# Kernel optimization log

Measured on AMD Instinct MI355X. Metric: run time of the kernel, lower is better.

The kernel has to match this reference:

```python
import jax, jax.numpy as jnp
import numpy as np

N_E = 1024
N_H = 16
SZ = N_E // N_H  # 64
NEG_INF = float('-inf')


def _layernorm(x, g, b):
    # Faithful to source: unbiased variance (ddof=1), eps added AFTER sqrt.
    mu = jnp.mean(x, axis=-1, keepdims=True)
    v = jnp.var(x, axis=-1, keepdims=True, ddof=1)
    xn = (x - mu) / (jnp.sqrt(v) + 1e-8)
    return g * xn + b


def setup_inputs() -> dict:
    key = jax.random.key(0)
    ks = jax.random.split(key, 16)
    s = 0.02
    x = jax.random.normal(ks[0], (4, 2048, N_E), dtype=jnp.float32)
    # Stacked per-head Q/K/V linears: weight [H, sz, n_e], bias [H, sz]
    Wq = jax.random.normal(ks[1], (N_H, SZ, N_E), dtype=jnp.float32) * s
    bq = jax.random.normal(ks[2], (N_H, SZ), dtype=jnp.float32) * s
    Wk = jax.random.normal(ks[3], (N_H, SZ, N_E), dtype=jnp.float32) * s
    bk = jax.random.normal(ks[4], (N_H, SZ), dtype=jnp.float32) * s
    Wv = jax.random.normal(ks[5], (N_H, SZ, N_E), dtype=jnp.float32) * s
    bv = jax.random.normal(ks[6], (N_H, SZ), dtype=jnp.float32) * s
    Wo = jax.random.normal(ks[7], (N_E, N_E), dtype=jnp.float32) * s
    bo = jax.random.normal(ks[8], (N_E,), dtype=jnp.float32) * s
    g1 = jnp.ones((N_E,), dtype=jnp.float32)
    be1 = jnp.zeros((N_E,), dtype=jnp.float32)
    g2 = jnp.ones((N_E,), dtype=jnp.float32)
    be2 = jnp.zeros((N_E,), dtype=jnp.float32)
    W1 = jax.random.normal(ks[9], (4 * N_E, N_E), dtype=jnp.float32) * s
    bf1 = jax.random.normal(ks[10], (4 * N_E,), dtype=jnp.float32) * s
    W2 = jax.random.normal(ks[11], (N_E, 4 * N_E), dtype=jnp.float32) * s
    bf2 = jax.random.normal(ks[12], (N_E,), dtype=jnp.float32) * s
    return dict(x=x, Wq=Wq, bq=bq, Wk=Wk, bk=bk, Wv=Wv, bv=bv, Wo=Wo, bo=bo,
                g1=g1, be1=be1, g2=g2, be2=be2, W1=W1, bf1=bf1, W2=W2, bf2=bf2)


def reference(x, Wq, bq, Wk, bk, Wv, bv, Wo, bo, g1, be1, g2, be2, W1, bf1, W2, bf2):
    # --- MHA sublayer ---
    xn = _layernorm(x, g1, be1)
    # Q/K/V for all heads at once: [B, H, S, sz]
    Q = jnp.einsum('bsd,hkd->bhsk', xn, Wq) + bq[None, :, None, :]
    K = jnp.einsum('bsd,hkd->bhsk', xn, Wk) + bk[None, :, None, :]
    V = jnp.einsum('bsd,hkd->bhsk', xn, Wv) + bv[None, :, None, :]
    scores = jnp.einsum('bhqk,bhmk->bhqm', Q, K) / (SZ ** 0.5)  # [B,H,S,S]
    # Faithful to source quirk: mask where tril(scores) == 0
    masked = jnp.where(jnp.tril(scores) == 0, NEG_INF, scores)
    attn = jax.nn.softmax(masked, axis=-1)
    o = jnp.einsum('bhqm,bhmk->bhqk', attn, V)  # [B,H,S,sz]
    B, H, S, _ = o.shape
    o = jnp.transpose(o, (0, 2, 1, 3)).reshape(B, S, H * SZ)  # concat heads
    x = x + o @ Wo.T + bo
    # --- FFN sublayer (dropout = identity in eval) ---
    xn2 = _layernorm(x, g2, be2)
    h = jax.nn.gelu(xn2 @ W1.T + bf1, approximate=False)
    x = x + h @ W2.T + bf2
    return x
```

## Files before the change

kernel.cpp:

```cpp
#include <hip/hip_runtime.h>
#include <math.h>


typedef unsigned short u16;
typedef unsigned int u32;
typedef __attribute__((ext_vector_type(8))) short bf16x8;
typedef __attribute__((ext_vector_type(4))) float f32x4;

#define T_TOK 8192
#define DM    1024
#define SEQ   2048
#define PST   88
#define TST   136

__device__ __forceinline__ u16 f2bf(float f) {
  union { float f; unsigned int u; } c; c.f = f;
  unsigned int u = c.u + 0x7fffu + ((c.u >> 16) & 1u);
  return (u16)(u >> 16);
}

__device__ __forceinline__ u32 pk2(float a, float b) {
  return (u32)f2bf(a) | ((u32)f2bf(b) << 16);
}

__device__ __forceinline__ float bf2f(short s) {
  union { float f; unsigned int u; } c; c.u = ((u32)(u16)s) << 16;
  return c.f;
}

__device__ __forceinline__ void gload16(const void* gp, void* lp) {
  __builtin_amdgcn_global_load_lds(
      (const __attribute__((address_space(1))) void*)gp,
      (__attribute__((address_space(3))) void*)lp, 16, 0, 0);
}

__device__ __forceinline__ float gelu_tanh(float v) {
  float u = 0.7978845608f * (v + 0.044715f * v * v * v);
  return v / (1.0f + __expf(-2.0f * u));
}

__global__ __launch_bounds__(256) void prep_kernel(
    const float* __restrict__ x, const float* __restrict__ g,
    const float* __restrict__ b, u16* __restrict__ xnB,
    const float* __restrict__ Wq, const float* __restrict__ Wk,
    const float* __restrict__ Wv, const float* __restrict__ Wo,
    const float* __restrict__ W1, const float* __restrict__ W2,
    u16* __restrict__ WqkvB, u16* __restrict__ WoB,
    u16* __restrict__ W1B, u16* __restrict__ W2B,
    const float* __restrict__ bq, const float* __restrict__ bk,
    const float* __restrict__ bv, float* __restrict__ bqkv) {
  __shared__ float red[4];
  const int bid = blockIdx.x, tid = threadIdx.x;
  if (bid < 8192) {
    const int l = tid & 63, w = tid >> 6;
    const size_t row = bid;
    float4 v = reinterpret_cast<const float4*>(x + row * DM)[tid];
    float s = v.x + v.y + v.z + v.w;
#pragma unroll
    for (int off = 1; off < 64; off <<= 1) s += __shfl_xor(s, off, 64);
    if (l == 0) red[w] = s;
    __syncthreads();
    float mu = (red[0] + red[1] + red[2] + red[3]) * (1.0f / 1024.0f);
    float dx = v.x - mu, dy = v.y - mu, dz = v.z - mu, dw = v.w - mu;
    float ss = dx * dx + dy * dy + dz * dz + dw * dw;
#pragma unroll
    for (int off = 1; off < 64; off <<= 1) ss += __shfl_xor(ss, off, 64);
    __syncthreads();
    if (l == 0) red[w] = ss;
    __syncthreads();
    float var = (red[0] + red[1] + red[2] + red[3]) * (1.0f / 1023.0f);
    float inv = 1.0f / (sqrtf(var) + 1e-8f);
    const int c = tid * 4;
    u16* o = xnB + row * DM + c;
    o[0] = f2bf(dx * inv * g[c + 0] + b[c + 0]);
    o[1] = f2bf(dy * inv * g[c + 1] + b[c + 1]);
    o[2] = f2bf(dz * inv * g[c + 2] + b[c + 2]);
    o[3] = f2bf(dw * inv * g[c + 3] + b[c + 3]);
  } else if (bid < 10240) {
    for (int i = (bid - 8192) * 256 + tid; i < 3145728; i += 2048 * 256) {
      const float* s; u16* d; int j;
      if (i < 262144)       { s = Wq; d = WqkvB;           j = i; }
      else if (i < 524288)  { s = Wk; d = WqkvB + 1048576; j = i - 262144; }
      else if (i < 786432)  { s = Wv; d = WqkvB + 2097152; j = i - 524288; }
      else if (i < 1048576) { s = Wo; d = WoB;             j = i - 786432; }
      else if (i < 2097152) { s = W1; d = W1B;             j = i - 1048576; }
      else                  { s = W2; d = W2B;             j = i - 2097152; }
      float4 v = reinterpret_cast<const float4*>(s)[j];
      ushort4 o = { f2bf(v.x), f2bf(v.y), f2bf(v.z), f2bf(v.w) };
      reinterpret_cast<ushort4*>(d)[j] = o;
    }
  } else {
    int i = (bid - 10240) * 256 + tid;
    float val = (i < 1024) ? bq[i] : (i < 2048) ? bk[i - 1024] : bv[i - 2048];
    bqkv[i] = val;
  }
}

__global__ __launch_bounds__(256) void ln_kernel_b(const u16* __restrict__ x,
    const float* __restrict__ g, const float* __restrict__ b, u16* __restrict__ out) {
  __shared__ float red[4];
  const int tid = threadIdx.x, l = tid & 63, w = tid >> 6;
  const size_t row = blockIdx.x;
  ushort4 raw = reinterpret_cast<const ushort4*>(x + row * DM)[tid];
  float vx = bf2f((short)raw.x), vy = bf2f((short)raw.y);
  float vz = bf2f((short)raw.z), vw = bf2f((short)raw.w);
  float s = vx + vy + vz + vw;
#pragma unroll
  for (int off = 1; off < 64; off <<= 1) s += __shfl_xor(s, off, 64);
  if (l == 0) red[w] = s;
  __syncthreads();
  float mu = (red[0] + red[1] + red[2] + red[3]) * (1.0f / 1024.0f);
  float dx = vx - mu, dy = vy - mu, dz = vz - mu, dw = vw - mu;
  float ss = dx * dx + dy * dy + dz * dz + dw * dw;
#pragma unroll
  for (int off = 1; off < 64; off <<= 1) ss += __shfl_xor(ss, off, 64);
  __syncthreads();
  if (l == 0) red[w] = ss;
  __syncthreads();
  float var = (red[0] + red[1] + red[2] + red[3]) * (1.0f / 1023.0f);
  float inv = 1.0f / (sqrtf(var) + 1e-8f);
  const int c = tid * 4;
  u16* o = out + row * DM + c;
  o[0] = f2bf(dx * inv * g[c + 0] + b[c + 0]);
  o[1] = f2bf(dy * inv * g[c + 1] + b[c + 1]);
  o[2] = f2bf(dz * inv * g[c + 2] + b[c + 2]);
  o[3] = f2bf(dw * inv * g[c + 3] + b[c + 3]);
}

template <int EPI, int BM>
__global__ __launch_bounds__(512) void gemm8p(const u16* __restrict__ A,
    const u16* __restrict__ Bw, const float* __restrict__ bias,
    const float* res, void* Cout, void* aux, int M, int N, int K, int gx) {
  constexpr int MI  = BM / 32;
  constexpr int AMI = MI / 2;
  constexpr int VC  = (BM == 256) ? 6 : 5;
  __shared__ __align__(16) u16 shm[BM * 128 + 256 * 128];
  const int tid = threadIdx.x;
  const int l = tid & 63;
  const int w = tid >> 6;
  const int wm = w >> 2, wn = w & 3;
  const int lr = l & 15, lg = l >> 4;

  const int nb = gridDim.x;
  const int q = nb >> 3, r = nb & 7;
  const int xcd = blockIdx.x & 7, jj = blockIdx.x >> 3;
  const int lid = (xcd < r ? xcd * (q + 1) : r * (q + 1) + (xcd - r) * q) + jj;
  const int stid = lid >> 5, pos = lid & 31;
  const int nstx = gx >> 2;
  const int stx = stid % nstx, sty = stid / nstx;
  const int bx = stx * 4 + (pos & 3), by = sty * 8 + (pos >> 2);
  const int m0 = by * BM, n0 = bx * 256;

  const int Dl = tid * 16;
  const int Ls = Dl ^ (((Dl >> 7) & 3) << 4);
  const int srow = Ls >> 6;
  const int scol = (Ls & 63) >> 1;
  const u16* aS0 = A  + (size_t)(m0 + srow) * K + scol;
  const u16* aS1 = aS0 + (size_t)128 * K;
  const u16* bS0 = Bw + (size_t)(n0 + srow) * K + scol;
  const u16* bS1 = bS0 + (size_t)128 * K;

  const int sx = ((lr >> 1) & 3) << 4;
  const int aBase = (wm * (BM / 2) + lr) * 64 + ((lg * 16) ^ sx);
  const int bBase = (wn * 64 + lr) * 64 + ((lg * 16) ^ sx);

  f32x4 acc[MI][4];
#pragma unroll
  for (int i = 0; i < MI; ++i)
#pragma unroll
    for (int j = 0; j < 4; ++j) acc[i][j] = f32x4{0.f, 0.f, 0.f, 0.f};
  bf16x8 bv[2][4];

  const int NT = K >> 6;
  const int NI = NT >> 1;

  auto stA = [&](int d, int ks, int tile) {
    u16* dst = shm + (d * 2 + ks) * (BM * 32) + tid * 8;
    const int ko = tile * 64 + ks * 32;
    gload16(aS0 + ko, dst);
    if constexpr (BM == 256) gload16(aS1 + ko, dst + 4096);
  };
  auto stB = [&](int d, int ks, int tile) {
    u16* dst = shm + BM * 128 + (d * 2 + ks) * (256 * 32) + tid * 8;
    const int ko = tile * 64 + ks * 32;
    gload16(bS0 + ko, dst);
    gload16(bS1 + ko, dst + 4096);
  };

  stB(0, 0, 0); stB(0, 1, 0); stA(0, 0, 0); stA(0, 1, 0);
  stB(1, 0, 1); stB(1, 1, 1); stA(1, 0, 1);
  asm volatile("s_waitcnt vmcnt(%0)" :: "i"(VC) : "memory");
  __builtin_amdgcn_sched_barrier(0);
  __builtin_amdgcn_s_barrier();

#define PHASE(DBUF, KS, MH, READB, STAGE, ENDV)                               \
  {                                                                           \
    const char* abuf = (const char*)(shm + ((DBUF) * 2 + (KS)) * (BM * 32));  \
    const char* bbuf =                                                        \
        (const char*)(shm + BM * 128 + ((DBUF) * 2 + (KS)) * (256 * 32));     \
    bf16x8 av[AMI];                                                           \
    _Pragma("unroll")                                                         \
    for (int i = 0; i < AMI; ++i)                                             \
      av[i] = *(const bf16x8*)(abuf + aBase + ((MH) * AMI + i) * 1024);       \
    if (READB) {                                                              \
      _Pragma("unroll")                                                       \
      for (int ni = 0; ni < 4; ++ni)                                          \
        bv[KS][ni] = *(const bf16x8*)(bbuf + bBase + ni * 1024);              \
    }                                                                         \
    STAGE;                                                                    \
    __builtin_amdgcn_s_barrier();                                             \
    asm volatile("s_waitcnt lgkmcnt(0)" ::: "memory");                        \
    __builtin_amdgcn_sched_barrier(0);                                        \
    __builtin_amdgcn_s_setprio(1);                                            \
    _Pragma("unroll")                                                         \
    for (int i = 0; i < AMI; ++i)                                             \
      _Pragma("unroll")                                                       \
      for (int ni = 0; ni < 4; ++ni)                                          \
        acc[(MH) * AMI + i][ni] = __builtin_amdgcn_mfma_f32_16x16x32_bf16(    \
            av[i], bv[KS][ni], acc[(MH) * AMI + i][ni], 0, 0, 0);             \
    __builtin_amdgcn_s_setprio(0);                                            \
    ENDV;                                                                     \
    __builtin_amdgcn_s_barrier();                                             \
  }

#define ENDV_CNT                                                              \
  {                                                                           \
    if (t + 1 < NI) {                                                         \
      asm volatile("s_waitcnt vmcnt(%0)" :: "i"(VC) : "memory");              \
    } else {                                                                  \
      asm volatile("s_waitcnt vmcnt(0)" ::: "memory");                        \
    }                                                                         \
    __builtin_amdgcn_sched_barrier(0);                                        \
  }

  for (int t = 0; t < NI; ++t) {
    const int t2 = 2 * t;
    const bool s0 = (t2 + 2 < NT);
    const bool s1 = (t2 + 3 < NT);
    PHASE(0, 0, 0, 1, { stA(1, 1, t2 + 1); }, {});
    PHASE(0, 1, 0, 1, { if (s0) stB(0, 0, t2 + 2); }, {});
    PHASE(0, 0, 1, 0, { if (s0) stB(0, 1, t2 + 2); }, {});
    PHASE(0, 1, 1, 0, { if (s0) stA(0, 0, t2 + 2); }, ENDV_CNT);
    PHASE(1, 0, 0, 1, { if (s0) stA(0, 1, t2 + 2); }, {});
    PHASE(1, 1, 0, 1, { if (s1) stB(1, 0, t2 + 3); }, {});
    PHASE(1, 0, 1, 0, { if (s1) stB(1, 1, t2 + 3); }, {});
    PHASE(1, 1, 1, 0, { if (s1) stA(1, 0, t2 + 3); }, ENDV_CNT);
  }
#undef PHASE
#undef ENDV_CNT

  float bs[4];
#pragma unroll
  for (int ni = 0; ni < 4; ++ni) bs[ni] = bias[n0 + wn * 64 + ni * 16 + lr];

  if constexpr (EPI == 0) {
    if (n0 >= 2048) {
      u16* ldsT = shm;
#pragma unroll
      for (int mi = 0; mi < MI; ++mi)
#pragma unroll
        for (int ni = 0; ni < 4; ++ni) {
          const int c = wn * 64 + ni * 16 + lr;
          const int r0 = wm * (BM / 2) + mi * 16 + lg * 4;
          ushort4 pk = { f2bf(acc[mi][ni][0] + bs[ni]),
                         f2bf(acc[mi][ni][1] + bs[ni]),
                         f2bf(acc[mi][ni][2] + bs[ni]),
                         f2bf(acc[mi][ni][3] + bs[ni]) };
          *(ushort4*)&ldsT[c * TST + r0] = pk;
        }
      __syncthreads();
      const int b0 = m0 >> 11, s0b = m0 & 2047;
      const int cc = tid >> 1, hf = tid & 1;
      const int hd = (n0 - 2048) + cc, hh = hd >> 6, dd = hd & 63;
      u16* dst = (u16*)aux +
                 (((size_t)(b0 * 16 + hh) * 64 + dd) << 11) + s0b + hf * 64;
      const u16* srcT = &ldsT[cc * TST + hf * 64];
#pragma unroll
      for (int i2 = 0; i2 < 8; ++i2)
        *(bf16x8*)(dst + i2 * 8) = *(const bf16x8*)(srcT + i2 * 8);
      return;
    }
  }

#pragma unroll
  for (int mi = 0; mi < MI; ++mi) {
#pragma unroll
    for (int j = 0; j < 4; ++j) {
      const int rr = m0 + wm * (BM / 2) + mi * 16 + lg * 4 + j;
#pragma unroll
      for (int ni = 0; ni < 4; ++ni) {
        const int c = n0 + wn * 64 + ni * 16 + lr;
        float v = acc[mi][ni][j] + bs[ni];
        if constexpr (EPI == 0) {
          ((u16*)Cout)[(size_t)rr * 2048 + c] = f2bf(v);
        } else if constexpr (EPI == 1) {
          const size_t idx = (size_t)rr * N + c;
          ((u16*)Cout)[idx] = f2bf(v + res[idx]);
        } else if constexpr (EPI == 2) {
          const size_t idx = (size_t)rr * N + c;
          ((u16*)Cout)[idx] = f2bf(gelu_tanh(v));
        } else {
          const size_t idx = (size_t)rr * N + c;
          ((float*)Cout)[idx] = v + bf2f((short)((const u16*)res)[idx]);
        }
      }
    }
  }
}

__global__ __launch_bounds__(512) void attn_kernel(const u16* __restrict__ qk,
    const u16* __restrict__ vt, u16* __restrict__ obuf) {
  __shared__ __align__(16) u16 ldsK[6][64 * 64];
  __shared__ __align__(16) u16 ldsV[6][64 * 64];
  __shared__ __align__(16) u16 ldsP[8][2][16 * PST];
  const int tid = threadIdx.x, l = tid & 63, w = tid >> 6;
  const int lr = l & 15, lg = l >> 4;
  const int lid = (blockIdx.x & 7) * 32 + (blockIdx.x >> 3);
  const int bh = lid >> 2, bx = lid & 3;
  const int b = bh >> 4, h = bh & 15;
  const u16* qbase = qk + (size_t)b * SEQ * 2048 + h * 64;
  const u16* kbase = qk + (size_t)b * SEQ * 2048 + 1024 + h * 64;
  const u16* vbase = vt + (size_t)bh * 64 * SEQ;

  const int srow = tid >> 3;
  const int scb  = ((tid & 7) * 16) ^ ((srow & 7) << 4);
  const int sel  = scb >> 1;

  auto stageKV = [&](int t) {
    const int bi = t % 6;
    gload16(kbase + (size_t)(t * 64 + srow) * 2048 + sel, &ldsK[bi][tid * 8]);
    gload16(vbase + (size_t)srow * SEQ + t * 64 + sel,    &ldsV[bi][tid * 8]);
  };

#pragma unroll
  for (int half = 0; half < 2; ++half) {
    const int qt = half ? (7 - bx) : bx;
    const int q0 = qt * 256 + w * 32;
    bf16x8 qf[2][2];
#pragma unroll
    for (int mi = 0; mi < 2; ++mi)
#pragma unroll
      for (int ks = 0; ks < 2; ++ks) {
        bf16x8 raw = *(const bf16x8*)(qbase +
            (size_t)(q0 + mi * 16 + lr) * 2048 + ks * 32 + lg * 8);
        bf16x8 sc8;
#pragma unroll
        for (int i = 0; i < 8; ++i) sc8[i] = (short)f2bf(bf2f(raw[i]) * 0.125f);
        qf[mi][ks] = sc8;
      }

    f32x4 o[2][4];
#pragma unroll
    for (int mi = 0; mi < 2; ++mi)
#pragma unroll
      for (int nd = 0; nd < 4; ++nd) o[mi][nd] = f32x4{0.f, 0.f, 0.f, 0.f};
    float m_[2] = {-1e30f, -1e30f}, ls[2] = {0.f, 0.f};

    const int nt = 4 * qt + 4;
    const int nip = nt >> 1;
    const int qmaxw = q0 + 31;

    stageKV(0); stageKV(1);

    for (int jt = 0; jt < nip; ++jt) {
      const int k0t = 2 * jt;
      if (jt + 1 < nip) {
        stageKV(k0t + 2); stageKV(k0t + 3);
        asm volatile("s_waitcnt vmcnt(4)" ::: "memory");
      } else {
        asm volatile("s_waitcnt vmcnt(0)" ::: "memory");
      }
      __builtin_amdgcn_s_barrier();
      __builtin_amdgcn_sched_barrier(0);

#pragma unroll
      for (int sub = 0; sub < 2; ++sub) {
        const int kt = k0t + sub;
        const u16* bK = &ldsK[kt % 6][0];
        const u16* bV = &ldsV[kt % 6][0];

        if (kt * 64 <= qmaxw) {
          f32x4 sc[2][4];
#pragma unroll
          for (int mi = 0; mi < 2; ++mi)
#pragma unroll
            for (int ni = 0; ni < 4; ++ni) sc[mi][ni] = f32x4{0.f, 0.f, 0.f, 0.f};
#pragma unroll
          for (int ks = 0; ks < 2; ++ks)
#pragma unroll
            for (int ni = 0; ni < 4; ++ni) {
              const int r2 = ni * 16 + lr;
              const int cb = (r2 << 7) + ((ks * 64 + lg * 16) ^ ((r2 & 7) << 4));
              bf16x8 kf = *(const bf16x8*)&bK[cb >> 1];
              sc[0][ni] = __builtin_amdgcn_mfma_f32_16x16x32_bf16(kf, qf[0][ks], sc[0][ni], 0, 0, 0);
              sc[1][ni] = __builtin_amdgcn_mfma_f32_16x16x32_bf16(kf, qf[1][ks], sc[1][ni], 0, 0, 0);
            }

          if (kt * 64 + 63 > q0) {
#pragma unroll
            for (int mi = 0; mi < 2; ++mi) {
              const int qa = q0 + mi * 16 + lr;
#pragma unroll
              for (int ni = 0; ni < 4; ++ni)
#pragma unroll
                for (int j = 0; j < 4; ++j) {
                  const int ka = kt * 64 + ni * 16 + lg * 4 + j;
                  if (ka > qa) sc[mi][ni][j] = -1e30f;
                }
            }
          }

#pragma unroll
          for (int mi = 0; mi < 2; ++mi) {
            float mx = sc[mi][0][0];
#pragma unroll
            for (int ni = 0; ni < 4; ++ni)
#pragma unroll
              for (int j = 0; j < 4; ++j) mx = fmaxf(mx, sc[mi][ni][j]);
            mx = fmaxf(mx, __shfl_xor(mx, 16, 64));
            mx = fmaxf(mx, __shfl_xor(mx, 32, 64));
            if (!__all(mx <= m_[mi] + 8.0f)) {
              const float newm = fmaxf(m_[mi], mx);
              const float alpha = __expf(m_[mi] - newm);
              m_[mi] = newm;
              ls[mi] *= alpha;
#pragma unroll
              for (int nd = 0; nd < 4; ++nd) {
                o[mi][nd][0] *= alpha; o[mi][nd][1] *= alpha;
                o[mi][nd][2] *= alpha; o[mi][nd][3] *= alpha;
              }
            }
            float ps = 0.f;
#pragma unroll
            for (int ni = 0; ni < 4; ++ni) {
              float p0 = __expf(sc[mi][ni][0] - m_[mi]);
              float p1 = __expf(sc[mi][ni][1] - m_[mi]);
              float p2 = __expf(sc[mi][ni][2] - m_[mi]);
              float p3 = __expf(sc[mi][ni][3] - m_[mi]);
              ps += (p0 + p1) + (p2 + p3);
              u32 w0 = pk2(p0, p1), w1 = pk2(p2, p3);
              *(uint2*)&ldsP[w][mi][lr * PST + ni * 16 + lg * 4] = make_uint2(w0, w1);
            }
            ps += __shfl_xor(ps, 16, 64);
            ps += __shfl_xor(ps, 32, 64);
            ls[mi] += ps;
          }

#pragma unroll
          for (int ks = 0; ks < 2; ++ks) {
            bf16x8 pf0 = *(const bf16x8*)&ldsP[w][0][lr * PST + ks * 32 + lg * 8];
            bf16x8 pf1 = *(const bf16x8*)&ldsP[w][1][lr * PST + ks * 32 + lg * 8];
#pragma unroll
            for (int nd = 0; nd < 4; ++nd) {
              const int r2 = nd * 16 + lr;
              const int cb = (r2 << 7) + ((ks * 64 + lg * 16) ^ ((r2 & 7) << 4));
              bf16x8 vf = *(const bf16x8*)&bV[cb >> 1];
              o[0][nd] = __builtin_amdgcn_mfma_f32_16x16x32_bf16(vf, pf0, o[0][nd], 0, 0, 0);
              o[1][nd] = __builtin_amdgcn_mfma_f32_16x16x32_bf16(vf, pf1, o[1][nd], 0, 0, 0);
            }
          }
        }
      }
    }
    __builtin_amdgcn_s_barrier();

#pragma unroll
    for (int mi = 0; mi < 2; ++mi) {
      const float inv = 1.0f / ls[mi];
      const int qrow = q0 + mi * 16 + lr;
      u16* op = obuf + (size_t)(b * SEQ + qrow) * DM + h * 64 + lg * 4;
#pragma unroll
      for (int nd = 0; nd < 4; ++nd) {
        ushort4 pk = { f2bf(o[mi][nd][0] * inv), f2bf(o[mi][nd][1] * inv),
                       f2bf(o[mi][nd][2] * inv), f2bf(o[mi][nd][3] * inv) };
        *(ushort4*)(op + nd * 16) = pk;
      }
    }
  }
}

extern "C" void kernel_launch(void* const* d_in, const int* in_sizes, int n_in,
                              void* d_out, int out_size, void* d_ws, size_t ws_size,
                              hipStream_t stream) {
  const float* x   = (const float*)d_in[0];
  const float* Wq  = (const float*)d_in[1];
  const float* bq  = (const float*)d_in[2];
  const float* Wk  = (const float*)d_in[3];
  const float* bk  = (const float*)d_in[4];
  const float* Wv  = (const float*)d_in[5];
  const float* bv  = (const float*)d_in[6];
  const float* Wo  = (const float*)d_in[7];
  const float* bo  = (const float*)d_in[8];
  const float* g1  = (const float*)d_in[9];
  const float* be1 = (const float*)d_in[10];
  const float* g2  = (const float*)d_in[11];
  const float* be2 = (const float*)d_in[12];
  const float* W1  = (const float*)d_in[13];
  const float* bf1 = (const float*)d_in[14];
  const float* W2  = (const float*)d_in[15];
  const float* bf2 = (const float*)d_in[16];
  float* out = (float*)d_out;

  char* ws = (char*)d_ws;
  size_t off = 0;
  auto alloc = [&](size_t bytes) {
    char* p = ws + off;
    off += (bytes + 255) & ~(size_t)255;
    return p;
  };
  u16* xnB = (u16*)alloc((size_t)T_TOK * DM * 2);
  u16* D    = (u16*)alloc((size_t)T_TOK * 4096 * 2);
  u16* qkB  = D;
  u16* VTg  = D + (size_t)T_TOK * 2048;
  u16* oB   = D + (size_t)T_TOK * 3072;
  u16* HB   = D;
  u16*   WqkvB = (u16*)alloc((size_t)3072 * 1024 * 2);
  u16*   WoB   = (u16*)alloc((size_t)1024 * 1024 * 2);
  u16*   W1B   = (u16*)alloc((size_t)4096 * 1024 * 2);
  u16*   W2B   = (u16*)alloc((size_t)1024 * 4096 * 2);
  u16*   x1B   = (u16*)alloc((size_t)T_TOK * DM * 2);
  float* bqkv  = (float*)alloc(3072 * 4);

  prep_kernel<<<10252, 256, 0, stream>>>(x, g1, be1, xnB,
                                         Wq, Wk, Wv, Wo, W1, W2,
                                         WqkvB, WoB, W1B, W2B,
                                         bq, bk, bv, bqkv);

  gemm8p<0, 128><<<768, 512, 0, stream>>>(xnB, WqkvB, bqkv, nullptr,
                                          qkB, VTg, T_TOK, 3072, 1024, 12);
  attn_kernel<<<256, 512, 0, stream>>>(qkB, VTg, oB);
  gemm8p<1, 128><<<256, 512, 0, stream>>>(oB, WoB, bo, x,
                                          x1B, nullptr, T_TOK, 1024, 1024, 4);

  ln_kernel_b<<<T_TOK, 256, 0, stream>>>(x1B, g2, be2, xnB);
  gemm8p<2, 256><<<512, 512, 0, stream>>>(xnB, W1B, bf1, nullptr,
                                          HB, nullptr, T_TOK, 4096, 1024, 16);
  gemm8p<3, 128><<<256, 512, 0, stream>>>(HB, W2B, bf2, (const float*)x1B,
                                          out, nullptr, T_TOK, 1024, 4096, 4);
}
```

Before: 344.6 us.

## Load K/V fragments directly from global memory instead of LDS staging

Drops the six-stage shared-memory ring buffer for K and V tiles, along with its async staging loads, waitcnt calls and workgroup barriers. Each wave now reads its K and V MFMA fragments straight from global memory, relying on L1/L2 caching for reuse across the 8 waves. This removes barrier synchronisation and LDS traffic, and each wave now breaks out at its own causal limit. In exchange it loses the prefetch pipelining and the sharing of loads across waves, which may expose global memory latency.

Measured after the change: 416.2 us. 20.8% more time.

```diff
diff --git a/kernel.cpp b/kernel.cpp
--- a/kernel.cpp
+++ b/kernel.cpp
@@ -310,8 +310,6 @@
 
 __global__ __launch_bounds__(512) void attn_kernel(const u16* __restrict__ qk,
     const u16* __restrict__ vt, u16* __restrict__ obuf) {
-  __shared__ __align__(16) u16 ldsK[6][64 * 64];
-  __shared__ __align__(16) u16 ldsV[6][64 * 64];
   __shared__ __align__(16) u16 ldsP[8][2][16 * PST];
   const int tid = threadIdx.x, l = tid & 63, w = tid >> 6;
   const int lr = l & 15, lg = l >> 4;
@@ -322,15 +320,7 @@
   const u16* kbase = qk + (size_t)b * SEQ * 2048 + 1024 + h * 64;
   const u16* vbase = vt + (size_t)bh * 64 * SEQ;
 
-  const int srow = tid >> 3;
-  const int scb  = ((tid & 7) * 16) ^ ((srow & 7) << 4);
-  const int sel  = scb >> 1;
-
-  auto stageKV = [&](int t) {
-    const int bi = t % 6;
-    gload16(kbase + (size_t)(t * 64 + srow) * 2048 + sel, &ldsK[bi][tid * 8]);
-    gload16(vbase + (size_t)srow * SEQ + t * 64 + sel,    &ldsV[bi][tid * 8]);
-  };
+  const int kcol = lg * 8;
 
 #pragma unroll
   for (int half = 0; half < 2; ++half) {
@@ -357,112 +347,91 @@
     float m_[2] = {-1e30f, -1e30f}, ls[2] = {0.f, 0.f};
 
     const int nt = 4 * qt + 4;
-    const int nip = nt >> 1;
     const int qmaxw = q0 + 31;
 
-    stageKV(0); stageKV(1);
-
-    for (int jt = 0; jt < nip; ++jt) {
-      const int k0t = 2 * jt;
-      if (jt + 1 < nip) {
-        stageKV(k0t + 2); stageKV(k0t + 3);
-        asm volatile("s_waitcnt vmcnt(4)" ::: "memory");
-      } else {
-        asm volatile("s_waitcnt vmcnt(0)" ::: "memory");
+    for (int kt = 0; kt < nt; ++kt) {
+      if (kt * 64 > qmaxw) break;
+
+      f32x4 sc[2][4];
+#pragma unroll
+      for (int mi = 0; mi < 2; ++mi)
+#pragma unroll
+        for (int ni = 0; ni < 4; ++ni) sc[mi][ni] = f32x4{0.f, 0.f, 0.f, 0.f};
+#pragma unroll
+      for (int ks = 0; ks < 2; ++ks)
+#pragma unroll
+        for (int ni = 0; ni < 4; ++ni) {
+          const int r2 = ni * 16 + lr;
+          bf16x8 kf = *(const bf16x8*)(kbase +
+              (size_t)(kt * 64 + r2) * 2048 + ks * 32 + kcol);
+          sc[0][ni] = __builtin_amdgcn_mfma_f32_16x16x32_bf16(kf, qf[0][ks], sc[0][ni], 0, 0, 0);
+          sc[1][ni] = __builtin_amdgcn_mfma_f32_16x16x32_bf16(kf, qf[1][ks], sc[1][ni], 0, 0, 0);
+        }
+
+      if (kt * 64 + 63 > q0) {
+#pragma unroll
+        for (int mi = 0; mi < 2; ++mi) {
+          const int qa = q0 + mi * 16 + lr;
+#pragma unroll
+          for (int ni = 0; ni < 4; ++ni)
+#pragma unroll
+            for (int j = 0; j < 4; ++j) {
+              const int ka = kt * 64 + ni * 16 + lg * 4 + j;
+              if (ka > qa) sc[mi][ni][j] = -1e30f;
+            }
+        }
       }
-      __builtin_amdgcn_s_barrier();
-      __builtin_amdgcn_sched_barrier(0);
-
-#pragma unroll
-      for (int sub = 0; sub < 2; ++sub) {
-        const int kt = k0t + sub;
-        const u16* bK = &ldsK[kt % 6][0];
-        const u16* bV = &ldsV[kt % 6][0];
-
-        if (kt * 64 <= qmaxw) {
-          f32x4 sc[2][4];
-#pragma unroll
-          for (int mi = 0; mi < 2; ++mi)
-#pragma unroll
-            for (int ni = 0; ni < 4; ++ni) sc[mi][ni] = f32x4{0.f, 0.f, 0.f, 0.f};
-#pragma unroll
-          for (int ks = 0; ks < 2; ++ks)
-#pragma unroll
-            for (int ni = 0; ni < 4; ++ni) {
-              const int r2 = ni * 16 + lr;
-              const int cb = (r2 << 7) + ((ks * 64 + lg * 16) ^ ((r2 & 7) << 4));
-              bf16x8 kf = *(const bf16x8*)&bK[cb >> 1];
-              sc[0][ni] = __builtin_amdgcn_mfma_f32_16x16x32_bf16(kf, qf[0][ks], sc[0][ni], 0, 0, 0);
-              sc[1][ni] = __builtin_amdgcn_mfma_f32_16x16x32_bf16(kf, qf[1][ks], sc[1][ni], 0, 0, 0);
-            }
-
-          if (kt * 64 + 63 > q0) {
-#pragma unroll
-            for (int mi = 0; mi < 2; ++mi) {
-              const int qa = q0 + mi * 16 + lr;
-#pragma unroll
-              for (int ni = 0; ni < 4; ++ni)
-#pragma unroll
-                for (int j = 0; j < 4; ++j) {
-                  const int ka = kt * 64 + ni * 16 + lg * 4 + j;
-                  if (ka > qa) sc[mi][ni][j] = -1e30f;
-                }
-            }
+
+#pragma unroll
+      for (int mi = 0; mi < 2; ++mi) {
+        float mx = sc[mi][0][0];
+#pragma unroll
+        for (int ni = 0; ni < 4; ++ni)
+#pragma unroll
+          for (int j = 0; j < 4; ++j) mx = fmaxf(mx, sc[mi][ni][j]);
+        mx = fmaxf(mx, __shfl_xor(mx, 16, 64));
+        mx = fmaxf(mx, __shfl_xor(mx, 32, 64));
+        if (!__all(mx <= m_[mi] + 8.0f)) {
+          const float newm = fmaxf(m_[mi], mx);
+          const float alpha = __expf(m_[mi] - newm);
+          m_[mi] = newm;
+          ls[mi] *= alpha;
+#pragma unroll
+          for (int nd = 0; nd < 4; ++nd) {
+            o[mi][nd][0] *= alpha; o[mi][nd][1] *= alpha;
+            o[mi][nd][2] *= alpha; o[mi][nd][3] *= alpha;
           }
-
-#pragma unroll
-          for (int mi = 0; mi < 2; ++mi) {
-            float mx = sc[mi][0][0];
-#pragma unroll
-            for (int ni = 0; ni < 4; ++ni)
-#pragma unroll
-              for (int j = 0; j < 4; ++j) mx = fmaxf(mx, sc[mi][ni][j]);
-            mx = fmaxf(mx, __shfl_xor(mx, 16, 64));
-            mx = fmaxf(mx, __shfl_xor(mx, 32, 64));
-            if (!__all(mx <= m_[mi] + 8.0f)) {
-              const float newm = fmaxf(m_[mi], mx);
-              const float alpha = __expf(m_[mi] - newm);
-              m_[mi] = newm;
-              ls[mi] *= alpha;
-#pragma unroll
-              for (int nd = 0; nd < 4; ++nd) {
-                o[mi][nd][0] *= alpha; o[mi][nd][1] *= alpha;
-                o[mi][nd][2] *= alpha; o[mi][nd][3] *= alpha;
-              }
-            }
-            float ps = 0.f;
-#pragma unroll
-            for (int ni = 0; ni < 4; ++ni) {
-              float p0 = __expf(sc[mi][ni][0] - m_[mi]);
-              float p1 = __expf(sc[mi][ni][1] - m_[mi]);
-              float p2 = __expf(sc[mi][ni][2] - m_[mi]);
-              float p3 = __expf(sc[mi][ni][3] - m_[mi]);
-              ps += (p0 + p1) + (p2 + p3);
-              u32 w0 = pk2(p0, p1), w1 = pk2(p2, p3);
-              *(uint2*)&ldsP[w][mi][lr * PST + ni * 16 + lg * 4] = make_uint2(w0, w1);
-            }
-            ps += __shfl_xor(ps, 16, 64);
-            ps += __shfl_xor(ps, 32, 64);
-            ls[mi] += ps;
-          }
-
-#pragma unroll
-          for (int ks = 0; ks < 2; ++ks) {
-            bf16x8 pf0 = *(const bf16x8*)&ldsP[w][0][lr * PST + ks * 32 + lg * 8];
-            bf16x8 pf1 = *(const bf16x8*)&ldsP[w][1][lr * PST + ks * 32 + lg * 8];
-#pragma unroll
-            for (int nd = 0; nd < 4; ++nd) {
-              const int r2 = nd * 16 + lr;
-              const int cb = (r2 << 7) + ((ks * 64 + lg * 16) ^ ((r2 & 7) << 4));
-              bf16x8 vf = *(const bf16x8*)&bV[cb >> 1];
-              o[0][nd] = __builtin_amdgcn_mfma_f32_16x16x32_bf16(vf, pf0, o[0][nd], 0, 0, 0);
-              o[1][nd] = __builtin_amdgcn_mfma_f32_16x16x32_bf16(vf, pf1, o[1][nd], 0, 0, 0);
-            }
-          }
+        }
+        float ps = 0.f;
+#pragma unroll
+        for (int ni = 0; ni < 4; ++ni) {
+          float p0 = __expf(sc[mi][ni][0] - m_[mi]);
+          float p1 = __expf(sc[mi][ni][1] - m_[mi]);
+          float p2 = __expf(sc[mi][ni][2] - m_[mi]);
+          float p3 = __expf(sc[mi][ni][3] - m_[mi]);
+          ps += (p0 + p1) + (p2 + p3);
+          u32 w0 = pk2(p0, p1), w1 = pk2(p2, p3);
+          *(uint2*)&ldsP[w][mi][lr * PST + ni * 16 + lg * 4] = make_uint2(w0, w1);
+        }
+        ps += __shfl_xor(ps, 16, 64);
+        ps += __shfl_xor(ps, 32, 64);
+        ls[mi] += ps;
+      }
+
+#pragma unroll
+      for (int ks = 0; ks < 2; ++ks) {
+        bf16x8 pf0 = *(const bf16x8*)&ldsP[w][0][lr * PST + ks * 32 + lg * 8];
+        bf16x8 pf1 = *(const bf16x8*)&ldsP[w][1][lr * PST + ks * 32 + lg * 8];
+#pragma unroll
+        for (int nd = 0; nd < 4; ++nd) {
+          const int r2 = nd * 16 + lr;
+          bf16x8 vf = *(const bf16x8*)(vbase +
+              (size_t)r2 * SEQ + kt * 64 + ks * 32 + kcol);
+          o[0][nd] = __builtin_amdgcn_mfma_f32_16x16x32_bf16(vf, pf0, o[0][nd], 0, 0, 0);
+          o[1][nd] = __builtin_amdgcn_mfma_f32_16x16x32_bf16(vf, pf1, o[1][nd], 0, 0, 0);
         }
       }
     }
-    __builtin_amdgcn_s_barrier();
 
 #pragma unroll
     for (int mi = 0; mi < 2; ++mi) {
```
